# Optimization experiments

Measured on AMD Instinct MI355X. Metric: run time of the kernel, lower is better.

The kernel has to match this reference:

```python
import jax, jax.numpy as jnp
import numpy as np

INPUT_SIZE = 40960
HIDDEN = 256
MAX_FEATS = 32
BATCH = 8192


def setup_inputs() -> dict:
    key = jax.random.key(0)
    ks = jax.random.split(key, 10)
    wf = jax.random.randint(ks[0], (BATCH, MAX_FEATS), 0, INPUT_SIZE, dtype=jnp.int64 if jax.config.jax_enable_x64 else jnp.int32)
    bf = jax.random.randint(ks[1], (BATCH, MAX_FEATS), 0, INPUT_SIZE, dtype=wf.dtype)
    pad_w = jax.random.uniform(ks[2], (BATCH, MAX_FEATS)) < 0.25
    pad_b = jax.random.uniform(ks[3], (BATCH, MAX_FEATS)) < 0.25
    wf = jnp.where(pad_w, -1, wf)
    bf = jnp.where(pad_b, -1, bf)
    stm = jax.random.bernoulli(ks[4], 0.5, (BATCH,)).astype(jnp.float32)
    # Parameters (torch Linear convention: weight [out, in]).
    bound = 1.0 / np.sqrt(INPUT_SIZE)
    ft_W = jax.random.uniform(ks[5], (HIDDEN, INPUT_SIZE), jnp.float32, -bound, bound)
    ft_b = jnp.zeros((HIDDEN,), jnp.float32)
    w1 = jax.random.normal(ks[6], (32, HIDDEN * 2), jnp.float32) * np.sqrt(2.0 / (HIDDEN * 2))
    b1 = jnp.zeros((32,), jnp.float32)
    w2 = jax.random.normal(ks[7], (32, 32), jnp.float32) * np.sqrt(2.0 / 32)
    b2 = jnp.zeros((32,), jnp.float32)
    wo = jax.random.uniform(ks[8], (1, 32), jnp.float32, -0.1, 0.1)
    bo = jnp.zeros((1,), jnp.float32)
    return {"white_features": wf, "black_features": bf, "stm": stm,
            "ft_W": ft_W, "ft_b": ft_b, "w1": w1, "b1": b1,
            "w2": w2, "b2": b2, "wo": wo, "bo": bo}


def _accumulate(idx, ft_Wt, ft_b):
    # idx: [B, F] with -1 padding; ft_Wt: [INPUT_SIZE, HIDDEN]
    valid = (idx >= 0)
    idxc = jnp.clip(idx, 0, INPUT_SIZE - 1)
    g = ft_Wt[idxc] * valid[..., None].astype(ft_Wt.dtype)  # [B, F, H]
    return g.sum(axis=1) + ft_b  # [B, H]


def reference(white_features, black_features, stm, ft_W, ft_b, w1, b1, w2, b2, wo, bo):
    ft_Wt = ft_W.T  # [INPUT_SIZE, HIDDEN]
    wh = _accumulate(white_features, ft_Wt, ft_b)
    bh = _accumulate(black_features, ft_Wt, ft_b)
    # clamp(relu(x), 0, 127) == clip(x, 0, 127)
    wh = jnp.clip(wh, 0.0, 127.0)
    bh = jnp.clip(bh, 0.0, 127.0)
    s = stm[:, None]
    us = s * wh + (1.0 - s) * bh
    them = s * bh + (1.0 - s) * wh
    x = jnp.concatenate([us, them], axis=1)  # [B, 2H]
    x = jax.nn.relu(x @ w1.T + b1)
    x = jax.nn.relu(x @ w2.T + b2)
    x = x @ wo.T + bo  # [B, 1]
    return jax.nn.sigmoid(x.squeeze(-1))
```

## Files before the change

kernel.cpp:

```cpp
#include <hip/hip_runtime.h>
#include <math.h>

#define BATCH   8192
#define HIDDEN  256
#define MAXF    32
#define ISZ     40960
#define TF      128

#define QSCALE  7.842927e-5f
#define INVQ    1.2750335e+4f
#define QOFF    (4096.0f * QSCALE)

__global__ __launch_bounds__(256) void transpose_q(const float* __restrict__ src,
                                                   unsigned char* __restrict__ dstq,
                                                   const float* __restrict__ w1,
                                                   const float* __restrict__ w2,
                                                   float* __restrict__ w1c,
                                                   float* __restrict__ w2t) {
    if (blockIdx.x == ISZ / TF) {
        for (int i = threadIdx.x; i < 32 * 512; i += 256) {
            int j = i >> 9, k = i & 511;
            w1c[(k >> 2) * 128 + j * 4 + (k & 3)] = w1[i];
        }
        for (int i = threadIdx.x; i < 32 * 32; i += 256) {
            int j = i >> 5, k = i & 31;
            w2t[k * 32 + j] = w2[i];
        }
        return;
    }

    __shared__ short tile[TF][260];
    const int t    = threadIdx.x;
    const int wave = t >> 6;
    const int lane = t & 63;
    const int F0   = blockIdx.x * TF;
    const int hw   = lane >> 5;
    const int l32  = lane & 31;

#pragma unroll 4
    for (int i = 0; i < 32; ++i) {
        const int h = i * 8 + wave * 2 + hw;
        const float4 v = *(const float4*)&src[(size_t)h * ISZ + F0 + 4 * l32];
        int q0 = __float2int_rn(v.x * INVQ); q0 = max(-127, min(127, q0)) + 128;
        int q1 = __float2int_rn(v.y * INVQ); q1 = max(-127, min(127, q1)) + 128;
        int q2 = __float2int_rn(v.z * INVQ); q2 = max(-127, min(127, q2)) + 128;
        int q3 = __float2int_rn(v.w * INVQ); q3 = max(-127, min(127, q3)) + 128;
        tile[4 * l32 + 0][h] = (short)q0;
        tile[4 * l32 + 1][h] = (short)q1;
        tile[4 * l32 + 2][h] = (short)q2;
        tile[4 * l32 + 3][h] = (short)q3;
    }
    __syncthreads();

    unsigned int* dq = (unsigned int*)dstq;
    for (int f = wave; f < TF; f += 4) {
        const short4 q = *(const short4*)&tile[f][4 * lane];
        unsigned int p = (q.x & 0xFF) | ((q.y & 0xFF) << 8) |
                         ((q.z & 0xFF) << 16) | ((unsigned int)(q.w & 0xFF) << 24);
        dq[(size_t)(F0 + f) * 64 + lane] = p;
    }
}

__global__ __launch_bounds__(256) void nnue_fused_q(
    const int* __restrict__ wf, const int* __restrict__ bfeat,
    const float* __restrict__ stm,
    const unsigned char* __restrict__ ftQ,
    const float* __restrict__ ftb,
    const float* __restrict__ w1c, const float* __restrict__ b1,
    const float* __restrict__ w2,  const float* __restrict__ b2,
    const float* __restrict__ wo,  const float* __restrict__ bo,
    float* __restrict__ out) {

    __shared__ int   sIdx[4][32][4];
    __shared__ float sX[8][512];
    __shared__ float sY1[8][32];
    __shared__ float sY2[8][32];

    const int t    = threadIdx.x;
    const int wave = t >> 6;
    const int lane = t & 63;
    const int g    = lane >> 4;
    const int c16  = lane & 15;
    const int ib0  = blockIdx.x * 8;

    {
        const int item = t >> 5, f = t & 31;
        sIdx[item >> 1][f][(item & 1) * 2 + 0] = wf   [(ib0 + item) * MAXF + f];
        sIdx[item >> 1][f][(item & 1) * 2 + 1] = bfeat[(ib0 + item) * MAXF + f];
    }
    __syncthreads();

    unsigned acc[8];
#pragma unroll
    for (int k = 0; k < 8; ++k) acc[k] = 0u;

    const uint4* T = (const uint4*)ftQ;

#pragma unroll 8
    for (int f = 0; f < MAXF; ++f) {
        const int idx = sIdx[wave][f][g];
        const int rc  = idx < 0 ? 0 : idx;
        uint4 d = T[rc * 16 + c16];
        if (idx < 0) { d.x = 0x80808080u; d.y = 0x80808080u;
                       d.z = 0x80808080u; d.w = 0x80808080u; }
        acc[0] += d.x & 0x00FF00FFu;  acc[1] += (d.x >> 8) & 0x00FF00FFu;
        acc[2] += d.y & 0x00FF00FFu;  acc[3] += (d.y >> 8) & 0x00FF00FFu;
        acc[4] += d.z & 0x00FF00FFu;  acc[5] += (d.z >> 8) & 0x00FF00FFu;
        acc[6] += d.w & 0x00FF00FFu;  acc[7] += (d.w >> 8) & 0x00FF00FFu;
    }

    const float4* ftb4 = (const float4*)ftb;
    float h[16];
#pragma unroll
    for (int m = 0; m < 4; ++m) {
        const float4 tb = ftb4[c16 * 4 + m];
        h[4*m+0] = (float)(acc[2*m]     & 0xFFFFu) * QSCALE + (tb.x - QOFF);
        h[4*m+1] = (float)(acc[2*m + 1] & 0xFFFFu) * QSCALE + (tb.y - QOFF);
        h[4*m+2] = (float)(acc[2*m]    >> 16)      * QSCALE + (tb.z - QOFF);
        h[4*m+3] = (float)(acc[2*m + 1] >> 16)     * QSCALE + (tb.w - QOFF);
    }
#pragma unroll
    for (int u = 0; u < 16; ++u) h[u] = fminf(fmaxf(h[u], 0.f), 127.f);

    const int   li  = wave * 2 + (g >> 1);
    const float s   = stm[ib0 + li];
    const int   off = (((g & 1) == 0) == (s > 0.5f)) ? 0 : 256;
    float* xrow = &sX[li][off + 16 * c16];
#pragma unroll
    for (int m = 0; m < 4; ++m)
        *(float4*)&xrow[4 * m] = make_float4(h[4*m], h[4*m+1], h[4*m+2], h[4*m+3]);
    __syncthreads();

    {
        const int j = t & 31, q = t >> 5;
        const float4* w1c4 = (const float4*)w1c;
        float y = b1[j];
#pragma unroll 4
        for (int ks = 0; ks < 128; ++ks) {
            const float4 x4 = *(const float4*)&sX[q][4 * ks];
            const float4 wv = w1c4[ks * 32 + j];
            y = fmaf(x4.x, wv.x, y); y = fmaf(x4.y, wv.y, y);
            y = fmaf(x4.z, wv.z, y); y = fmaf(x4.w, wv.w, y);
        }
        sY1[q][j] = fmaxf(y, 0.0f);
    }
    __syncthreads();

    {
        const int j = t & 31, q = t >> 5;
        float y = b2[j];
#pragma unroll
        for (int k = 0; k < 32; ++k) y = fmaf(sY1[q][k], w2[k * 32 + j], y);
        sY2[q][j] = fmaxf(y, 0.0f);
    }
    __syncthreads();

    if (t < 8) {
        float y = bo[0];
#pragma unroll
        for (int k = 0; k < 32; ++k) y = fmaf(sY2[t][k], wo[k], y);
        out[ib0 + t] = 1.0f / (1.0f + expf(-y));
    }
}

__global__ __launch_bounds__(256) void nnue_fused_fb(
    const int* __restrict__ wf, const int* __restrict__ bfeat,
    const float* __restrict__ stm,
    const float* __restrict__ ftW, const float* __restrict__ ftb,
    const float* __restrict__ w1, const float* __restrict__ b1,
    const float* __restrict__ w2, const float* __restrict__ b2,
    const float* __restrict__ wo, const float* __restrict__ bo,
    float* __restrict__ out) {

    __shared__ float sX[4][512];
    __shared__ float sP[2][4][32];
    __shared__ float sY2[4][32];

    const int t = threadIdx.x, wave = t >> 6, lane = t & 63;
    const int b = blockIdx.x * 4 + wave;
    int myidx = (lane < 32) ? wf[b * MAXF + lane] : bfeat[b * MAXF + (lane - 32)];
    const float4* ftb4 = (const float4*)ftb;
    float4 accw = ftb4[lane];
    float4 accb = accw;

    for (int f = 0; f < MAXF; ++f) {
        int iw = __builtin_amdgcn_readlane(myidx, f);
        int ib = __builtin_amdgcn_readlane(myidx, f + 32);
        float mw = (iw >= 0) ? 1.0f : 0.0f;
        float mb = (ib >= 0) ? 1.0f : 0.0f;
        int iwc = iw < 0 ? 0 : iw;
        int ibc = ib < 0 ? 0 : ib;
#pragma unroll
        for (int c = 0; c < 4; ++c) {
            float gw = ftW[(size_t)(4 * lane + c) * ISZ + iwc];
            float gb = ftW[(size_t)(4 * lane + c) * ISZ + ibc];
            float* aw = (c == 0) ? &accw.x : (c == 1) ? &accw.y : (c == 2) ? &accw.z : &accw.w;
            float* ab = (c == 0) ? &accb.x : (c == 1) ? &accb.y : (c == 2) ? &accb.z : &accb.w;
            *aw = fmaf(gw, mw, *aw);
            *ab = fmaf(gb, mb, *ab);
        }
    }
#pragma unroll
    for (int c = 0; c < 4; ++c) {
        float* aw = (c == 0) ? &accw.x : (c == 1) ? &accw.y : (c == 2) ? &accw.z : &accw.w;
        float* ab = (c == 0) ? &accb.x : (c == 1) ? &accb.y : (c == 2) ? &accb.z : &accb.w;
        *aw = fminf(fmaxf(*aw, 0.f), 127.f);
        *ab = fminf(fmaxf(*ab, 0.f), 127.f);
    }
    float s = stm[b];
    float4 us, th;
    if (s > 0.5f) { us = accw; th = accb; } else { us = accb; th = accw; }
    ((float4*)sX[wave])[lane] = us;
    ((float4*)sX[wave])[64 + lane] = th;
    __syncthreads();
    {
        const int j = t & 31, q = (t >> 5) & 3, kh = t >> 7;
        const float* x = sX[q];
        float y = kh ? 0.0f : b1[j];
        const int k0 = kh * 256;
        for (int kk = 0; kk < 256; ++kk) {
            const int k = k0 + kk;
            y = fmaf(x[k], w1[j * 512 + k], y);
        }
        sP[kh][q][j] = y;
    }
    __syncthreads();
    if (t < 128) {
        const int q = t >> 5, j = t & 31;
        float y = b2[j];
        for (int k = 0; k < 32; ++k) {
            float x1 = fmaxf(sP[0][q][k] + sP[1][q][k], 0.0f);
            y = fmaf(x1, w2[j * 32 + k], y);
        }
        sY2[q][j] = fmaxf(y, 0.0f);
    }
    __syncthreads();
    if (t < 4) {
        float y = bo[0];
        for (int k = 0; k < 32; ++k) y = fmaf(sY2[t][k], wo[k], y);
        out[blockIdx.x * 4 + t] = 1.0f / (1.0f + expf(-y));
    }
}

extern "C" void kernel_launch(void* const* d_in, const int* in_sizes, int n_in,
                              void* d_out, int out_size, void* d_ws, size_t ws_size,
                              hipStream_t stream) {
    const int*   wf  = (const int*)d_in[0];
    const int*   bfe = (const int*)d_in[1];
    const float* stm = (const float*)d_in[2];
    const float* ftW = (const float*)d_in[3];
    const float* ftb = (const float*)d_in[4];
    const float* w1  = (const float*)d_in[5];
    const float* b1  = (const float*)d_in[6];
    const float* w2  = (const float*)d_in[7];
    const float* b2  = (const float*)d_in[8];
    const float* wo  = (const float*)d_in[9];
    const float* bo  = (const float*)d_in[10];
    float* out = (float*)d_out;

    const size_t ftQ_bytes = (size_t)ISZ * HIDDEN;
    const size_t w1c_bytes = 512 * 32 * 4;
    const size_t w2t_bytes = 32 * 32 * 4;
    const size_t need      = ftQ_bytes + w1c_bytes + w2t_bytes;

    if (ws_size >= need) {
        unsigned char* ftQ = (unsigned char*)d_ws;
        float* w1c = (float*)((char*)d_ws + ftQ_bytes);
        float* w2t = w1c + 512 * 32;
        transpose_q<<<ISZ / TF + 1, 256, 0, stream>>>(ftW, ftQ, w1, w2, w1c, w2t);
        nnue_fused_q<<<BATCH / 8, 256, 0, stream>>>(
            wf, bfe, stm, ftQ, ftb, w1c, b1, w2t, b2, wo, bo, out);
    } else {
        nnue_fused_fb<<<BATCH / 4, 256, 0, stream>>>(
            wf, bfe, stm, ftW, ftb, w1, b1, w2, b2, wo, bo, out);
    }
}
```

Measured before the change: 132.8 us.

## Fuse weight quantize-transpose and inference into one cooperative kernel with grid sync

Merges the per-call quantize/transpose of the feature-transformer weights and the fused NNUE inference into a single cooperative kernel launched with 1024 blocks, separated by a grid-wide barrier. Each block first quantizes 32-feature tiles of ft_W through shared memory into the uint8 table, one block also repacks w1/w2, then all blocks run the gather-accumulate and MLP. This removes one kernel launch and the gap between kernels, at the cost of a grid sync and a requirement that all 1024 blocks be co-resident. If the cooperative launch fails, it falls back to the previous two-kernel path.

```diff
diff --git a/kernel.cpp b/kernel.cpp
--- a/kernel.cpp
+++ b/kernel.cpp
@@ -1,15 +1,170 @@
 #include <hip/hip_runtime.h>
+#include <hip/hip_cooperative_groups.h>
 #include <math.h>
+
+namespace cg = cooperative_groups;
 
 #define BATCH   8192
 #define HIDDEN  256
 #define MAXF    32
 #define ISZ     40960
 #define TF      128
+#define TF2     32
 
 #define QSCALE  7.842927e-5f
 #define INVQ    1.2750335e+4f
 #define QOFF    (4096.0f * QSCALE)
+
+__global__ __launch_bounds__(256) void nnue_mega(
+    const int* __restrict__ wf, const int* __restrict__ bfeat,
+    const float* __restrict__ stm,
+    const float* __restrict__ ftW, const float* __restrict__ ftb,
+    const float* __restrict__ w1,  const float* __restrict__ b1,
+    const float* __restrict__ w2s, const float* __restrict__ b2,
+    const float* __restrict__ wo,  const float* __restrict__ bo,
+    unsigned char* __restrict__ ftQ, float* __restrict__ w1c,
+    float* __restrict__ w2t, float* __restrict__ out) {
+
+    __shared__ union {
+        short tile[TF2][260];
+        struct {
+            int   sIdx[4][32][4];
+            float sX[8][512];
+            float sY1[8][32];
+            float sY2[8][32];
+        } g;
+    } sm;
+
+    const int t    = threadIdx.x;
+    const int wave = t >> 6;
+    const int lane = t & 63;
+
+    const int ib0   = blockIdx.x * 8;
+    const int item8 = t >> 5;
+    const int ff    = t & 31;
+    const int idxW  = wf   [(ib0 + item8) * MAXF + ff];
+    const int idxB  = bfeat[(ib0 + item8) * MAXF + ff];
+
+    unsigned int* dq = (unsigned int*)ftQ;
+    for (int c = blockIdx.x; c < ISZ / TF2; c += gridDim.x) {
+        const int F0 = c * TF2;
+#pragma unroll
+        for (int i = 0; i < 8; ++i) {
+            const int h  = i * 32 + wave * 8 + (lane >> 3);
+            const int fb = 4 * (lane & 7);
+            const float4 v = *(const float4*)&ftW[(size_t)h * ISZ + F0 + fb];
+            int q0 = __float2int_rn(v.x * INVQ); q0 = max(-127, min(127, q0)) + 128;
+            int q1 = __float2int_rn(v.y * INVQ); q1 = max(-127, min(127, q1)) + 128;
+            int q2 = __float2int_rn(v.z * INVQ); q2 = max(-127, min(127, q2)) + 128;
+            int q3 = __float2int_rn(v.w * INVQ); q3 = max(-127, min(127, q3)) + 128;
+            sm.tile[fb + 0][h] = (short)q0;
+            sm.tile[fb + 1][h] = (short)q1;
+            sm.tile[fb + 2][h] = (short)q2;
+            sm.tile[fb + 3][h] = (short)q3;
+        }
+        __syncthreads();
+#pragma unroll
+        for (int f = wave; f < TF2; f += 4) {
+            const short4 q = *(const short4*)&sm.tile[f][4 * lane];
+            unsigned int p = (q.x & 0xFF) | ((q.y & 0xFF) << 8) |
+                             ((q.z & 0xFF) << 16) | ((unsigned int)(q.w & 0xFF) << 24);
+            dq[(size_t)(F0 + f) * 64 + lane] = p;
+        }
+        __syncthreads();
+    }
+    if (blockIdx.x == 512) {
+        for (int i = t; i < 32 * 512; i += 256) {
+            int j = i >> 9, k = i & 511;
+            w1c[(k >> 2) * 128 + j * 4 + (k & 3)] = w1[i];
+        }
+        for (int i = t; i < 32 * 32; i += 256) {
+            int j = i >> 5, k = i & 31;
+            w2t[k * 32 + j] = w2s[i];
+        }
+    }
+
+    __threadfence();
+    cg::this_grid().sync();
+
+    const int g   = lane >> 4;
+    const int c16 = lane & 15;
+
+    sm.g.sIdx[item8 >> 1][ff][(item8 & 1) * 2 + 0] = idxW;
+    sm.g.sIdx[item8 >> 1][ff][(item8 & 1) * 2 + 1] = idxB;
+    __syncthreads();
+
+    unsigned acc[8];
+#pragma unroll
+    for (int k = 0; k < 8; ++k) acc[k] = 0u;
+
+    const uint4* T = (const uint4*)ftQ;
+
+#pragma unroll 8
+    for (int f = 0; f < MAXF; ++f) {
+        const int idx = sm.g.sIdx[wave][f][g];
+        const int rc  = idx < 0 ? 0 : idx;
+        uint4 d = T[rc * 16 + c16];
+        if (idx < 0) { d.x = 0x80808080u; d.y = 0x80808080u;
+                       d.z = 0x80808080u; d.w = 0x80808080u; }
+        acc[0] += d.x & 0x00FF00FFu;  acc[1] += (d.x >> 8) & 0x00FF00FFu;
+        acc[2] += d.y & 0x00FF00FFu;  acc[3] += (d.y >> 8) & 0x00FF00FFu;
+        acc[4] += d.z & 0x00FF00FFu;  acc[5] += (d.z >> 8) & 0x00FF00FFu;
+        acc[6] += d.w & 0x00FF00FFu;  acc[7] += (d.w >> 8) & 0x00FF00FFu;
+    }
+
+    const float4* ftb4 = (const float4*)ftb;
+    float h[16];
+#pragma unroll
+    for (int m = 0; m < 4; ++m) {
+        const float4 tb = ftb4[c16 * 4 + m];
+        h[4*m+0] = (float)(acc[2*m]     & 0xFFFFu) * QSCALE + (tb.x - QOFF);
+        h[4*m+1] = (float)(acc[2*m + 1] & 0xFFFFu) * QSCALE + (tb.y - QOFF);
+        h[4*m+2] = (float)(acc[2*m]    >> 16)      * QSCALE + (tb.z - QOFF);
+        h[4*m+3] = (float)(acc[2*m + 1] >> 16)     * QSCALE + (tb.w - QOFF);
+    }
+#pragma unroll
+    for (int u = 0; u < 16; ++u) h[u] = fminf(fmaxf(h[u], 0.f), 127.f);
+
+    const int   li  = wave * 2 + (g >> 1);
+    const float s   = stm[ib0 + li];
+    const int   off = (((g & 1) == 0) == (s > 0.5f)) ? 0 : 256;
+    float* xrow = &sm.g.sX[li][off + 16 * c16];
+#pragma unroll
+    for (int m = 0; m < 4; ++m)
+        *(float4*)&xrow[4 * m] = make_float4(h[4*m], h[4*m+1], h[4*m+2], h[4*m+3]);
+    __syncthreads();
+
+    {
+        const int j = t & 31, q = t >> 5;
+        const float4* w1c4 = (const float4*)w1c;
+        float y = b1[j];
+#pragma unroll 4
+        for (int ks = 0; ks < 128; ++ks) {
+            const float4 x4 = *(const float4*)&sm.g.sX[q][4 * ks];
+            const float4 wv = w1c4[ks * 32 + j];
+            y = fmaf(x4.x, wv.x, y); y = fmaf(x4.y, wv.y, y);
+            y = fmaf(x4.z, wv.z, y); y = fmaf(x4.w, wv.w, y);
+        }
+        sm.g.sY1[q][j] = fmaxf(y, 0.0f);
+    }
+    __syncthreads();
+
+    {
+        const int j = t & 31, q = t >> 5;
+        float y = b2[j];
+#pragma unroll
+        for (int k = 0; k < 32; ++k) y = fmaf(sm.g.sY1[q][k], w2t[k * 32 + j], y);
+        sm.g.sY2[q][j] = fmaxf(y, 0.0f);
+    }
+    __syncthreads();
+
+    if (t < 8) {
+        float y = bo[0];
+#pragma unroll
+        for (int k = 0; k < 32; ++k) y = fmaf(sm.g.sY2[t][k], wo[k], y);
+        out[ib0 + t] = 1.0f / (1.0f + expf(-y));
+    }
+}
 
 __global__ __launch_bounds__(256) void transpose_q(const float* __restrict__ src,
                                                    unsigned char* __restrict__ dstq,
@@ -267,9 +422,19 @@
         unsigned char* ftQ = (unsigned char*)d_ws;
         float* w1c = (float*)((char*)d_ws + ftQ_bytes);
         float* w2t = w1c + 512 * 32;
-        transpose_q<<<ISZ / TF + 1, 256, 0, stream>>>(ftW, ftQ, w1, w2, w1c, w2t);
-        nnue_fused_q<<<BATCH / 8, 256, 0, stream>>>(
-            wf, bfe, stm, ftQ, ftb, w1c, b1, w2t, b2, wo, bo, out);
+
+        void* kargs[] = {
+            (void*)&wf, (void*)&bfe, (void*)&stm, (void*)&ftW, (void*)&ftb,
+            (void*)&w1, (void*)&b1,  (void*)&w2,  (void*)&b2,  (void*)&wo,
+            (void*)&bo, (void*)&ftQ, (void*)&w1c, (void*)&w2t, (void*)&out
+        };
+        hipError_t e = hipLaunchCooperativeKernel(
+            (const void*)nnue_mega, dim3(BATCH / 8), dim3(256), kargs, 0, stream);
+        if (e != hipSuccess) {
+            transpose_q<<<ISZ / TF + 1, 256, 0, stream>>>(ftW, ftQ, w1, w2, w1c, w2t);
+            nnue_fused_q<<<BATCH / 8, 256, 0, stream>>>(
+                wf, bfe, stm, ftQ, ftb, w1c, b1, w2t, b2, wo, bo, out);
+        }
     } else {
         nnue_fused_fb<<<BATCH / 4, 256, 0, stream>>>(
             wf, bfe, stm, ftW, ftb, w1, b1, w2, b2, wo, bo, out);
```

Result: slower. 294.2 us (+121.6%).

## Shrink transpose tiles, add sentinel pad row, batch gather loads, use perm unpack

Applied to the files above, without the earlier changes.

The quantize-transpose kernel now processes 32 features per block instead of 128, launching many more blocks for better occupancy. It also writes an extra all-0x80 sentinel row so padded indices can load that row rather than being masked after the load. The accumulation loop issues eight independent gathers before consuming them, giving more memory-level parallelism, and replaces the mask/shift byte unpacking with v_perm byte selects. The cost is a slightly larger workspace and higher register pressure from holding eight uint4 values in flight.

```diff
diff --git a/kernel.cpp b/kernel.cpp
--- a/kernel.cpp
+++ b/kernel.cpp
@@ -5,19 +5,24 @@
 #define HIDDEN  256
 #define MAXF    32
 #define ISZ     40960
-#define TF      128
+#define TF2     32
 
 #define QSCALE  7.842927e-5f
 #define INVQ    1.2750335e+4f
 #define QOFF    (4096.0f * QSCALE)
 
-__global__ __launch_bounds__(256) void transpose_q(const float* __restrict__ src,
-                                                   unsigned char* __restrict__ dstq,
-                                                   const float* __restrict__ w1,
-                                                   const float* __restrict__ w2,
-                                                   float* __restrict__ w1c,
-                                                   float* __restrict__ w2t) {
-    if (blockIdx.x == ISZ / TF) {
+#define SEL_EVEN 0x00060004u
+#define SEL_ODD  0x00070005u
+
+__global__ __launch_bounds__(256) void transpose_q32(const float* __restrict__ src,
+                                                     unsigned char* __restrict__ dstq,
+                                                     const float* __restrict__ w1,
+                                                     const float* __restrict__ w2,
+                                                     float* __restrict__ w1c,
+                                                     float* __restrict__ w2t) {
+    unsigned int* dq = (unsigned int*)dstq;
+
+    if (blockIdx.x == ISZ / TF2) {
         for (int i = threadIdx.x; i < 32 * 512; i += 256) {
             int j = i >> 9, k = i & 511;
             w1c[(k >> 2) * 128 + j * 4 + (k & 3)] = w1[i];
@@ -26,34 +31,35 @@
             int j = i >> 5, k = i & 31;
             w2t[k * 32 + j] = w2[i];
         }
+        if (threadIdx.x < 64)
+            dq[(size_t)ISZ * 64 + threadIdx.x] = 0x80808080u;
         return;
     }
 
-    __shared__ short tile[TF][260];
+    __shared__ short tile[TF2][260];
     const int t    = threadIdx.x;
     const int wave = t >> 6;
     const int lane = t & 63;
-    const int F0   = blockIdx.x * TF;
-    const int hw   = lane >> 5;
-    const int l32  = lane & 31;
-
-#pragma unroll 4
-    for (int i = 0; i < 32; ++i) {
-        const int h = i * 8 + wave * 2 + hw;
-        const float4 v = *(const float4*)&src[(size_t)h * ISZ + F0 + 4 * l32];
+    const int F0   = blockIdx.x * TF2;
+
+#pragma unroll
+    for (int i = 0; i < 8; ++i) {
+        const int h  = i * 32 + wave * 8 + (lane >> 3);
+        const int fb = 4 * (lane & 7);
+        const float4 v = *(const float4*)&src[(size_t)h * ISZ + F0 + fb];
         int q0 = __float2int_rn(v.x * INVQ); q0 = max(-127, min(127, q0)) + 128;
         int q1 = __float2int_rn(v.y * INVQ); q1 = max(-127, min(127, q1)) + 128;
         int q2 = __float2int_rn(v.z * INVQ); q2 = max(-127, min(127, q2)) + 128;
         int q3 = __float2int_rn(v.w * INVQ); q3 = max(-127, min(127, q3)) + 128;
-        tile[4 * l32 + 0][h] = (short)q0;
-        tile[4 * l32 + 1][h] = (short)q1;
-        tile[4 * l32 + 2][h] = (short)q2;
-        tile[4 * l32 + 3][h] = (short)q3;
-    }
-    __syncthreads();
-
-    unsigned int* dq = (unsigned int*)dstq;
-    for (int f = wave; f < TF; f += 4) {
+        tile[fb + 0][h] = (short)q0;
+        tile[fb + 1][h] = (short)q1;
+        tile[fb + 2][h] = (short)q2;
+        tile[fb + 3][h] = (short)q3;
+    }
+    __syncthreads();
+
+#pragma unroll
+    for (int f = wave; f < TF2; f += 4) {
         const short4 q = *(const short4*)&tile[f][4 * lane];
         unsigned int p = (q.x & 0xFF) | ((q.y & 0xFF) << 8) |
                          ((q.z & 0xFF) << 16) | ((unsigned int)(q.w & 0xFF) << 24);
@@ -94,19 +100,28 @@
 #pragma unroll
     for (int k = 0; k < 8; ++k) acc[k] = 0u;
 
-    const uint4* T = (const uint4*)ftQ;
-
-#pragma unroll 8
-    for (int f = 0; f < MAXF; ++f) {
-        const int idx = sIdx[wave][f][g];
-        const int rc  = idx < 0 ? 0 : idx;
-        uint4 d = T[rc * 16 + c16];
-        if (idx < 0) { d.x = 0x80808080u; d.y = 0x80808080u;
-                       d.z = 0x80808080u; d.w = 0x80808080u; }
-        acc[0] += d.x & 0x00FF00FFu;  acc[1] += (d.x >> 8) & 0x00FF00FFu;
-        acc[2] += d.y & 0x00FF00FFu;  acc[3] += (d.y >> 8) & 0x00FF00FFu;
-        acc[4] += d.z & 0x00FF00FFu;  acc[5] += (d.z >> 8) & 0x00FF00FFu;
-        acc[6] += d.w & 0x00FF00FFu;  acc[7] += (d.w >> 8) & 0x00FF00FFu;
+    const uint4* Tl = (const uint4*)ftQ + c16;
+
+#pragma unroll
+    for (int fb = 0; fb < 4; ++fb) {
+        uint4 d[8];
+#pragma unroll
+        for (int u = 0; u < 8; ++u) {
+            const int idx = sIdx[wave][fb * 8 + u][g];
+            const int rc  = idx < 0 ? ISZ : idx;
+            d[u] = Tl[(size_t)rc * 16];
+        }
+#pragma unroll
+        for (int u = 0; u < 8; ++u) {
+            acc[0] += __builtin_amdgcn_perm(d[u].x, 0u, SEL_EVEN);
+            acc[1] += __builtin_amdgcn_perm(d[u].x, 0u, SEL_ODD);
+            acc[2] += __builtin_amdgcn_perm(d[u].y, 0u, SEL_EVEN);
+            acc[3] += __builtin_amdgcn_perm(d[u].y, 0u, SEL_ODD);
+            acc[4] += __builtin_amdgcn_perm(d[u].z, 0u, SEL_EVEN);
+            acc[5] += __builtin_amdgcn_perm(d[u].z, 0u, SEL_ODD);
+            acc[6] += __builtin_amdgcn_perm(d[u].w, 0u, SEL_EVEN);
+            acc[7] += __builtin_amdgcn_perm(d[u].w, 0u, SEL_ODD);
+        }
     }
 
     const float4* ftb4 = (const float4*)ftb;
@@ -258,7 +273,7 @@
     const float* bo  = (const float*)d_in[10];
     float* out = (float*)d_out;
 
-    const size_t ftQ_bytes = (size_t)ISZ * HIDDEN;
+    const size_t ftQ_bytes = (size_t)(ISZ + 1) * HIDDEN;
     const size_t w1c_bytes = 512 * 32 * 4;
     const size_t w2t_bytes = 32 * 32 * 4;
     const size_t need      = ftQ_bytes + w1c_bytes + w2t_bytes;
@@ -267,7 +282,7 @@
         unsigned char* ftQ = (unsigned char*)d_ws;
         float* w1c = (float*)((char*)d_ws + ftQ_bytes);
         float* w2t = w1c + 512 * 32;
-        transpose_q<<<ISZ / TF + 1, 256, 0, stream>>>(ftW, ftQ, w1, w2, w1c, w2t);
+        transpose_q32<<<ISZ / TF2 + 1, 256, 0, stream>>>(ftW, ftQ, w1, w2, w1c, w2t);
         nnue_fused_q<<<BATCH / 8, 256, 0, stream>>>(
             wf, bfe, stm, ftQ, ftb, w1c, b1, w2t, b2, wo, bo, out);
     } else {
```

Measured after the change: 133.9 us. No clear change (+0.8%).
